# Optimization experiments

Hardware: AMD Instinct MI355X
Metric: run time of the kernel (lower is better)

The kernel has to match this reference:

```python
import jax, jax.numpy as jnp
import numpy as np

NUM_HEAD = 16
DIM_Q = 1024
DIM_K = 1024
DIM_KEY = 64
DIM_VAL = 64
EPS = 1e-6


def setup_inputs() -> dict:
    key = jax.random.key(0)
    ks = jax.random.split(key, 9)
    B, S = 4, 2048
    q = jax.random.normal(ks[0], (B, S, DIM_Q), dtype=jnp.float32)
    k = jax.random.normal(ks[1], (B, S, DIM_K), dtype=jnp.float32)
    v = jax.random.normal(ks[2], (B, S, DIM_K), dtype=jnp.float32)
    # Linear(in, out) weights stored as [out, in] like torch; applied as x @ W.T
    w_q = jax.random.normal(ks[3], (NUM_HEAD * DIM_KEY, DIM_Q), dtype=jnp.float32) * (1.0 / np.sqrt(DIM_Q))
    w_k = jax.random.normal(ks[4], (NUM_HEAD * DIM_KEY, DIM_K), dtype=jnp.float32) * (1.0 / np.sqrt(DIM_K))
    w_v = jax.random.normal(ks[5], (NUM_HEAD * DIM_KEY, DIM_K), dtype=jnp.float32) * (1.0 / np.sqrt(DIM_K))
    w_fc = jax.random.normal(ks[6], (DIM_Q, NUM_HEAD * DIM_VAL), dtype=jnp.float32) * (1.0 / np.sqrt(NUM_HEAD * DIM_VAL))
    ln_gamma = jnp.ones((DIM_Q,), dtype=jnp.float32)
    ln_beta = jnp.zeros((DIM_Q,), dtype=jnp.float32)
    return {"q": q, "k": k, "v": v, "w_q": w_q, "w_k": w_k, "w_v": w_v,
            "w_fc": w_fc, "ln_gamma": ln_gamma, "ln_beta": ln_beta}


def _layer_norm(x, gamma, beta):
    mu = jnp.mean(x, axis=-1, keepdims=True)
    var = jnp.mean(jnp.square(x - mu), axis=-1, keepdims=True)
    return (x - mu) * jax.lax.rsqrt(var + EPS) * gamma + beta


def reference(q, k, v, w_q, w_k, w_v, w_fc, ln_gamma, ln_beta):
    B, Sq, _ = q.shape
    Sk = k.shape[1]
    residual = q
    # projections -> [B, H, S, D]
    qh = (q @ w_q.T).reshape(B, Sq, NUM_HEAD, DIM_KEY).transpose(0, 2, 1, 3)
    kh = (k @ w_k.T).reshape(B, Sk, NUM_HEAD, DIM_KEY).transpose(0, 2, 1, 3)
    vh = (v @ w_v.T).reshape(B, Sk, NUM_HEAD, DIM_VAL).transpose(0, 2, 1, 3)
    scale = 1.0 / np.sqrt(DIM_KEY).astype(np.float32)
    attn = jax.nn.softmax(jnp.einsum('bhqd,bhkd->bhqk', qh, kh) * scale, axis=-1)
    out = jnp.einsum('bhqk,bhkd->bhqd', attn, vh)  # [B,H,Sq,Dv]
    out = out.transpose(0, 2, 1, 3).reshape(B, Sq, NUM_HEAD * DIM_VAL)
    out = out @ w_fc.T
    out = _layer_norm(out + residual, ln_gamma, ln_beta)
    return out, attn
```

## Files before the change

### kernel.cpp

```cpp
#include <hip/hip_runtime.h>


typedef __bf16 bf16_t;
typedef __bf16 bf16x4 __attribute__((ext_vector_type(4)));
typedef __bf16 bf16x8 __attribute__((ext_vector_type(8)));
typedef float f32x4 __attribute__((ext_vector_type(4)));

#define MFMA16(a, b, c) __builtin_amdgcn_mfma_f32_16x16x32_bf16((a), (b), (c), 0, 0, 0)

__global__ __launch_bounds__(256) void gemm_xwT(
    const float* __restrict__ A, const float* __restrict__ W,
    void* __restrict__ out, int mode, float scale)
{
    constexpr int K = 1024;
    __shared__ bf16_t As[128][72];
    __shared__ bf16_t Ws[128][72];

    const int t    = threadIdx.x;
    const int lane = t & 63;
    const int wv   = t >> 6;
    const int m0   = blockIdx.y * 128;
    const int n0   = blockIdx.x * 128;
    const int wr   = (wv >> 1) * 64;
    const int wc   = (wv & 1) * 64;

    f32x4 acc[4][4] = {};

    const int fr = lane & 15;
    const int fk = (lane >> 4) << 3;

    for (int k0 = 0; k0 < K; k0 += 64) {
        __syncthreads();
        for (int i = 0; i < 8; ++i) {
            int slot = t + i * 256;
            int r    = slot >> 4;
            int cg   = (slot & 15) << 2;
            float4 av = *(const float4*)(A + (size_t)(m0 + r) * K + k0 + cg);
            float4 wvv = *(const float4*)(W + (size_t)(n0 + r) * K + k0 + cg);
            bf16x4 ab, wb;
            ab[0] = (bf16_t)av.x;  ab[1] = (bf16_t)av.y;
            ab[2] = (bf16_t)av.z;  ab[3] = (bf16_t)av.w;
            wb[0] = (bf16_t)wvv.x; wb[1] = (bf16_t)wvv.y;
            wb[2] = (bf16_t)wvv.z; wb[3] = (bf16_t)wvv.w;
            *(bf16x4*)&As[r][cg] = ab;
            *(bf16x4*)&Ws[r][cg] = wb;
        }
        __syncthreads();
        for (int ks = 0; ks < 2; ++ks) {
            const int kk = ks * 32 + fk;
            bf16x8 af[4], bw[4];
            for (int i = 0; i < 4; ++i) af[i] = *(const bf16x8*)&As[wr + i * 16 + fr][kk];
            for (int j = 0; j < 4; ++j) bw[j] = *(const bf16x8*)&Ws[wc + j * 16 + fr][kk];
            for (int i = 0; i < 4; ++i)
                for (int j = 0; j < 4; ++j)
                    acc[i][j] = MFMA16(af[i], bw[j], acc[i][j]);
        }
    }

    const int cq = lane & 15;
    const int rq = (lane >> 4) << 2;
    for (int i = 0; i < 4; ++i) {
        for (int j = 0; j < 4; ++j) {
            const int n = n0 + wc + j * 16 + cq;
            for (int r = 0; r < 4; ++r) {
                const int m = m0 + wr + i * 16 + rq + r;
                const float v = acc[i][j][r] * scale;
                if (mode == 0) {
                    const int b = m >> 11, s = m & 2047;
                    const int h = n >> 6,  d = n & 63;
                    ((bf16_t*)out)[((size_t)((b * 16 + h) * 2048 + s) << 6) + d] = (bf16_t)v;
                } else {
                    ((float*)out)[(size_t)m * 1024 + n] = v;
                }
            }
        }
    }
}

__global__ __launch_bounds__(256) void attn_kernel(
    const bf16_t* __restrict__ qh, const bf16_t* __restrict__ kh,
    const bf16_t* __restrict__ vh, float* __restrict__ attn_out,
    float* __restrict__ o_out)
{
    __shared__ bf16_t Qs[64][72];
    __shared__ bf16_t Ks[128][72];
    __shared__ bf16_t Vt[64][136];
    __shared__ bf16_t Ps[64][136];
    __shared__ float  Linv[64];

    const int t    = threadIdx.x;
    const int lane = t & 63;
    const int wv   = t >> 6;
    const int qt   = blockIdx.x;
    const int bh   = blockIdx.y;
    const int sq0  = qt * 64;
    const size_t hbase = (size_t)bh * 2048 * 64;

    for (int i = 0; i < 2; ++i) {
        int slot = t + i * 256;
        int r = slot >> 3, g = (slot & 7) << 3;
        *(bf16x8*)&Qs[r][g] = *(const bf16x8*)(qh + hbase + (size_t)(sq0 + r) * 64 + g);
    }
    __syncthreads();

    const int fr    = lane & 15;
    const int fk    = (lane >> 4) << 3;
    const int rq    = (lane >> 4) << 2;
    const int rbase = wv * 16;

    const bf16x8 qa0 = *(const bf16x8*)&Qs[rbase + fr][fk];
    const bf16x8 qa1 = *(const bf16x8*)&Qs[rbase + fr][32 + fk];

    float lsum[4] = {0.f, 0.f, 0.f, 0.f};
    for (int kt = 0; kt < 16; ++kt) {
        __syncthreads();
        for (int i = 0; i < 4; ++i) {
            int slot = t + i * 256;
            int r = slot >> 3, g = (slot & 7) << 3;
            *(bf16x8*)&Ks[r][g] =
                *(const bf16x8*)(kh + hbase + (size_t)(kt * 128 + r) * 64 + g);
        }
        __syncthreads();
        for (int ct = 0; ct < 8; ++ct) {
            f32x4 c = {0.f, 0.f, 0.f, 0.f};
            bf16x8 b0 = *(const bf16x8*)&Ks[ct * 16 + fr][fk];
            bf16x8 b1 = *(const bf16x8*)&Ks[ct * 16 + fr][32 + fk];
            c = MFMA16(qa0, b0, c);
            c = MFMA16(qa1, b1, c);
            lsum[0] += __expf(c[0]); lsum[1] += __expf(c[1]);
            lsum[2] += __expf(c[2]); lsum[3] += __expf(c[3]);
        }
    }
    for (int m = 1; m < 16; m <<= 1)
        for (int r = 0; r < 4; ++r)
            lsum[r] += __shfl_xor(lsum[r], m, 64);
    if ((lane & 15) == 0)
        for (int r = 0; r < 4; ++r)
            Linv[rbase + rq + r] = 1.0f / lsum[r];
    __syncthreads();
    float inv[4];
    for (int r = 0; r < 4; ++r) inv[r] = Linv[rbase + rq + r];

    f32x4 oacc[4] = {};
    for (int kt = 0; kt < 16; ++kt) {
        __syncthreads();
        for (int i = 0; i < 4; ++i) {
            int slot = t + i * 256;
            int r = slot >> 3, g = (slot & 7) << 3;
            *(bf16x8*)&Ks[r][g] =
                *(const bf16x8*)(kh + hbase + (size_t)(kt * 128 + r) * 64 + g);
            int n = t & 127;
            int dvg = ((t >> 7) + 2 * i) << 3;
            bf16x8 vv = *(const bf16x8*)(vh + hbase + (size_t)(kt * 128 + n) * 64 + dvg);
            for (int j = 0; j < 8; ++j) Vt[dvg + j][n] = vv[j];
        }
        __syncthreads();
        for (int ct = 0; ct < 8; ++ct) {
            f32x4 c = {0.f, 0.f, 0.f, 0.f};
            bf16x8 b0 = *(const bf16x8*)&Ks[ct * 16 + fr][fk];
            bf16x8 b1 = *(const bf16x8*)&Ks[ct * 16 + fr][32 + fk];
            c = MFMA16(qa0, b0, c);
            c = MFMA16(qa1, b1, c);
            for (int r = 0; r < 4; ++r) {
                float p = __expf(c[r]) * inv[r];
                Ps[rbase + rq + r][ct * 16 + fr] = (bf16_t)p;
            }
        }
        __syncthreads();
        const size_t abase = ((size_t)bh * 2048 + sq0) * 2048 + kt * 128;
        for (int i = 0; i < 8; ++i) {
            int slot = t + i * 256;
            int r = slot >> 5, cg = (slot & 31) << 2;
            bf16x4 pv = *(const bf16x4*)&Ps[r][cg];
            float4 f;
            f.x = (float)pv[0]; f.y = (float)pv[1];
            f.z = (float)pv[2]; f.w = (float)pv[3];
            *(float4*)(attn_out + abase + (size_t)r * 2048 + cg) = f;
        }
        bf16x8 pa[4];
        for (int ks = 0; ks < 4; ++ks)
            pa[ks] = *(const bf16x8*)&Ps[rbase + fr][ks * 32 + fk];
        for (int dt = 0; dt < 4; ++dt)
            for (int ks = 0; ks < 4; ++ks) {
                bf16x8 bv = *(const bf16x8*)&Vt[dt * 16 + fr][ks * 32 + fk];
                oacc[dt] = MFMA16(pa[ks], bv, oacc[dt]);
            }
    }

    {
        const int b = bh >> 4, h = bh & 15;
        for (int dt = 0; dt < 4; ++dt)
            for (int r = 0; r < 4; ++r) {
                const int m = sq0 + rbase + rq + r;
                const int dv = dt * 16 + fr;
                o_out[(size_t)(b * 2048 + m) * 1024 + h * 64 + dv] = oacc[dt][r];
            }
    }
}

__global__ __launch_bounds__(256) void ln_kernel(
    const float* __restrict__ x, const float* __restrict__ resid,
    const float* __restrict__ gamma, const float* __restrict__ beta,
    float* __restrict__ out)
{
    const int row = blockIdx.x;
    const int t   = threadIdx.x;
    const size_t base = (size_t)row * 1024 + t * 4;
    float4 v = *(const float4*)(x + base);
    float4 rz = *(const float4*)(resid + base);
    v.x += rz.x; v.y += rz.y; v.z += rz.z; v.w += rz.w;
    float s  = v.x + v.y + v.z + v.w;
    float sq = v.x * v.x + v.y * v.y + v.z * v.z + v.w * v.w;
    for (int m = 1; m < 64; m <<= 1) {
        s  += __shfl_xor(s, m, 64);
        sq += __shfl_xor(sq, m, 64);
    }
    __shared__ float ws_s[4], ws_q[4];
    const int wv = t >> 6;
    if ((t & 63) == 0) { ws_s[wv] = s; ws_q[wv] = sq; }
    __syncthreads();
    s  = ws_s[0] + ws_s[1] + ws_s[2] + ws_s[3];
    sq = ws_q[0] + ws_q[1] + ws_q[2] + ws_q[3];
    const float mu  = s * (1.0f / 1024.0f);
    const float var = sq * (1.0f / 1024.0f) - mu * mu;
    const float rs  = rsqrtf(var + 1e-6f);
    float4 g = *(const float4*)(gamma + t * 4);
    float4 b = *(const float4*)(beta + t * 4);
    float4 y;
    y.x = (v.x - mu) * rs * g.x + b.x;
    y.y = (v.y - mu) * rs * g.y + b.y;
    y.z = (v.z - mu) * rs * g.z + b.z;
    y.w = (v.w - mu) * rs * g.w + b.w;
    *(float4*)(out + base) = y;
}

extern "C" void kernel_launch(void* const* d_in, const int* in_sizes, int n_in,
                              void* d_out, int out_size, void* d_ws, size_t ws_size,
                              hipStream_t stream)
{
    const float* q       = (const float*)d_in[0];
    const float* k       = (const float*)d_in[1];
    const float* v       = (const float*)d_in[2];
    const float* w_q     = (const float*)d_in[3];
    const float* w_k     = (const float*)d_in[4];
    const float* w_v     = (const float*)d_in[5];
    const float* w_fc    = (const float*)d_in[6];
    const float* ln_g    = (const float*)d_in[7];
    const float* ln_b    = (const float*)d_in[8];

    float* out      = (float*)d_out;
    float* attn_out = out + (size_t)4 * 2048 * 1024;

    char* ws = (char*)d_ws;
    bf16_t* qh    = (bf16_t*)(ws);
    bf16_t* kh    = (bf16_t*)(ws + (size_t)16777216);
    bf16_t* vh    = (bf16_t*)(ws + (size_t)33554432);
    float*  o_f32 = (float*)(ws + (size_t)50331648);
    float*  fc    = (float*)(ws);

    dim3 gg(8, 64);
    gemm_xwT<<<gg, 256, 0, stream>>>(q, w_q, qh, 0, 0.125f);
    gemm_xwT<<<gg, 256, 0, stream>>>(k, w_k, kh, 0, 1.0f);
    gemm_xwT<<<gg, 256, 0, stream>>>(v, w_v, vh, 0, 1.0f);

    attn_kernel<<<dim3(32, 64), 256, 0, stream>>>(qh, kh, vh, attn_out, o_f32);

    gemm_xwT<<<gg, 256, 0, stream>>>(o_f32, w_fc, fc, 1, 1.0f);

    ln_kernel<<<8192, 256, 0, stream>>>(fc, q, ln_g, ln_b, out);
}
```

Measured before the change: 1.545 ms.

## Enlarge attention query tile, pre-transpose V in projection, write attn directly from registers

The attention kernel now processes 128 query rows per block (32 per wave, two MFMA fragments), so each K/V tile loaded into shared memory is reused across twice as many queries. The V projection writes V already transposed (head, dim, seq), which removes the per-element scatter transpose into shared memory. Score MFMAs are issued with swapped operands so each lane holds four consecutive keys, letting attention probabilities be written to global memory as float4 directly from registers instead of through a shared-memory staging pass. The softmax row-sum reduction shrinks to two shuffles, and the Linv shared buffer and its barrier are removed. Loops are also explicitly unrolled. The larger tile raises register and LDS use per block and halves the grid, which may reduce occupancy.

Measured after the change: 1.683 ms. 1.09x slower.

```diff
diff --git a/kernel.cpp b/kernel.cpp
--- a/kernel.cpp
+++ b/kernel.cpp
@@ -31,11 +31,12 @@
 
     for (int k0 = 0; k0 < K; k0 += 64) {
         __syncthreads();
+        #pragma unroll
         for (int i = 0; i < 8; ++i) {
             int slot = t + i * 256;
             int r    = slot >> 4;
             int cg   = (slot & 15) << 2;
-            float4 av = *(const float4*)(A + (size_t)(m0 + r) * K + k0 + cg);
+            float4 av  = *(const float4*)(A + (size_t)(m0 + r) * K + k0 + cg);
             float4 wvv = *(const float4*)(W + (size_t)(n0 + r) * K + k0 + cg);
             bf16x4 ab, wb;
             ab[0] = (bf16_t)av.x;  ab[1] = (bf16_t)av.y;
@@ -46,12 +47,17 @@
             *(bf16x4*)&Ws[r][cg] = wb;
         }
         __syncthreads();
+        #pragma unroll
         for (int ks = 0; ks < 2; ++ks) {
             const int kk = ks * 32 + fk;
             bf16x8 af[4], bw[4];
+            #pragma unroll
             for (int i = 0; i < 4; ++i) af[i] = *(const bf16x8*)&As[wr + i * 16 + fr][kk];
+            #pragma unroll
             for (int j = 0; j < 4; ++j) bw[j] = *(const bf16x8*)&Ws[wc + j * 16 + fr][kk];
+            #pragma unroll
             for (int i = 0; i < 4; ++i)
+                #pragma unroll
                 for (int j = 0; j < 4; ++j)
                     acc[i][j] = MFMA16(af[i], bw[j], acc[i][j]);
         }
@@ -59,19 +65,32 @@
 
     const int cq = lane & 15;
     const int rq = (lane >> 4) << 2;
+    #pragma unroll
     for (int i = 0; i < 4; ++i) {
+        #pragma unroll
         for (int j = 0; j < 4; ++j) {
-            const int n = n0 + wc + j * 16 + cq;
-            for (int r = 0; r < 4; ++r) {
-                const int m = m0 + wr + i * 16 + rq + r;
-                const float v = acc[i][j][r] * scale;
-                if (mode == 0) {
+            const int n  = n0 + wc + j * 16 + cq;
+            const int mb = m0 + wr + i * 16 + rq;
+            if (mode == 0) {
+                const int h = n >> 6, d = n & 63;
+                #pragma unroll
+                for (int r = 0; r < 4; ++r) {
+                    const int m = mb + r;
                     const int b = m >> 11, s = m & 2047;
-                    const int h = n >> 6,  d = n & 63;
-                    ((bf16_t*)out)[((size_t)((b * 16 + h) * 2048 + s) << 6) + d] = (bf16_t)v;
-                } else {
-                    ((float*)out)[(size_t)m * 1024 + n] = v;
+                    ((bf16_t*)out)[((size_t)((b * 16 + h) * 2048 + s) << 6) + d] =
+                        (bf16_t)(acc[i][j][r] * scale);
                 }
+            } else if (mode == 1) {
+                #pragma unroll
+                for (int r = 0; r < 4; ++r)
+                    ((float*)out)[(size_t)(mb + r) * 1024 + n] = acc[i][j][r] * scale;
+            } else {
+                const int b = mb >> 11, s = mb & 2047;
+                const int h = n >> 6, d = n & 63;
+                bf16x4 pv;
+                #pragma unroll
+                for (int r = 0; r < 4; ++r) pv[r] = (bf16_t)(acc[i][j][r] * scale);
+                *(bf16x4*)((bf16_t*)out + (((size_t)(b * 16 + h) * 64 + d) << 11) + s) = pv;
             }
         }
     }
@@ -79,122 +98,147 @@
 
 __global__ __launch_bounds__(256) void attn_kernel(
     const bf16_t* __restrict__ qh, const bf16_t* __restrict__ kh,
-    const bf16_t* __restrict__ vh, float* __restrict__ attn_out,
+    const bf16_t* __restrict__ vt, float* __restrict__ attn_out,
     float* __restrict__ o_out)
 {
-    __shared__ bf16_t Qs[64][72];
     __shared__ bf16_t Ks[128][72];
     __shared__ bf16_t Vt[64][136];
-    __shared__ bf16_t Ps[64][136];
-    __shared__ float  Linv[64];
+    __shared__ bf16_t Ps[128][136];
 
     const int t    = threadIdx.x;
     const int lane = t & 63;
     const int wv   = t >> 6;
     const int qt   = blockIdx.x;
     const int bh   = blockIdx.y;
-    const int sq0  = qt * 64;
-    const size_t hbase = (size_t)bh * 2048 * 64;
-
-    for (int i = 0; i < 2; ++i) {
-        int slot = t + i * 256;
-        int r = slot >> 3, g = (slot & 7) << 3;
-        *(bf16x8*)&Qs[r][g] = *(const bf16x8*)(qh + hbase + (size_t)(sq0 + r) * 64 + g);
+    const int sq0  = qt * 128;
+    const size_t hbase  = (size_t)bh * 2048 * 64;
+    const size_t vtbase = (size_t)bh * 64 * 2048;
+
+    const int fr    = lane & 15;
+    const int quad  = lane >> 4;
+    const int fk    = quad << 3;
+    const int qbase = wv * 32;
+
+    {
+        const int r0 = t >> 3, g = (t & 7) << 3;
+        #pragma unroll
+        for (int i = 0; i < 4; ++i) {
+            int r = r0 + i * 32;
+            *(bf16x8*)&Ps[r][g] = *(const bf16x8*)(qh + hbase + (size_t)(sq0 + r) * 64 + g);
+        }
     }
     __syncthreads();
-
-    const int fr    = lane & 15;
-    const int fk    = (lane >> 4) << 3;
-    const int rq    = (lane >> 4) << 2;
-    const int rbase = wv * 16;
-
-    const bf16x8 qa0 = *(const bf16x8*)&Qs[rbase + fr][fk];
-    const bf16x8 qa1 = *(const bf16x8*)&Qs[rbase + fr][32 + fk];
-
-    float lsum[4] = {0.f, 0.f, 0.f, 0.f};
+    bf16x8 qa[2][2];
+    #pragma unroll
+    for (int f = 0; f < 2; ++f)
+        #pragma unroll
+        for (int h2 = 0; h2 < 2; ++h2)
+            qa[f][h2] = *(const bf16x8*)&Ps[qbase + f * 16 + fr][h2 * 32 + fk];
+
+    float lsum[2] = {0.f, 0.f};
     for (int kt = 0; kt < 16; ++kt) {
         __syncthreads();
-        for (int i = 0; i < 4; ++i) {
-            int slot = t + i * 256;
-            int r = slot >> 3, g = (slot & 7) << 3;
-            *(bf16x8*)&Ks[r][g] =
-                *(const bf16x8*)(kh + hbase + (size_t)(kt * 128 + r) * 64 + g);
-        }
-        __syncthreads();
+        {
+            const int r0 = t >> 3, g = (t & 7) << 3;
+            #pragma unroll
+            for (int i = 0; i < 4; ++i) {
+                int r = r0 + i * 32;
+                *(bf16x8*)&Ks[r][g] =
+                    *(const bf16x8*)(kh + hbase + (size_t)(kt * 128 + r) * 64 + g);
+            }
+        }
+        __syncthreads();
+        #pragma unroll
         for (int ct = 0; ct < 8; ++ct) {
-            f32x4 c = {0.f, 0.f, 0.f, 0.f};
             bf16x8 b0 = *(const bf16x8*)&Ks[ct * 16 + fr][fk];
             bf16x8 b1 = *(const bf16x8*)&Ks[ct * 16 + fr][32 + fk];
-            c = MFMA16(qa0, b0, c);
-            c = MFMA16(qa1, b1, c);
-            lsum[0] += __expf(c[0]); lsum[1] += __expf(c[1]);
-            lsum[2] += __expf(c[2]); lsum[3] += __expf(c[3]);
-        }
-    }
-    for (int m = 1; m < 16; m <<= 1)
-        for (int r = 0; r < 4; ++r)
-            lsum[r] += __shfl_xor(lsum[r], m, 64);
-    if ((lane & 15) == 0)
-        for (int r = 0; r < 4; ++r)
-            Linv[rbase + rq + r] = 1.0f / lsum[r];
-    __syncthreads();
-    float inv[4];
-    for (int r = 0; r < 4; ++r) inv[r] = Linv[rbase + rq + r];
-
-    f32x4 oacc[4] = {};
+            #pragma unroll
+            for (int f = 0; f < 2; ++f) {
+                f32x4 c = {0.f, 0.f, 0.f, 0.f};
+                c = MFMA16(b0, qa[f][0], c);
+                c = MFMA16(b1, qa[f][1], c);
+                lsum[f] += __expf(c[0]) + __expf(c[1]) + __expf(c[2]) + __expf(c[3]);
+            }
+        }
+    }
+    float inv[2];
+    #pragma unroll
+    for (int f = 0; f < 2; ++f) {
+        float s = lsum[f];
+        s += __shfl_xor(s, 16, 64);
+        s += __shfl_xor(s, 32, 64);
+        inv[f] = 1.0f / s;
+    }
+
+    f32x4 oacc[2][4] = {};
     for (int kt = 0; kt < 16; ++kt) {
         __syncthreads();
-        for (int i = 0; i < 4; ++i) {
-            int slot = t + i * 256;
-            int r = slot >> 3, g = (slot & 7) << 3;
-            *(bf16x8*)&Ks[r][g] =
-                *(const bf16x8*)(kh + hbase + (size_t)(kt * 128 + r) * 64 + g);
-            int n = t & 127;
-            int dvg = ((t >> 7) + 2 * i) << 3;
-            bf16x8 vv = *(const bf16x8*)(vh + hbase + (size_t)(kt * 128 + n) * 64 + dvg);
-            for (int j = 0; j < 8; ++j) Vt[dvg + j][n] = vv[j];
-        }
-        __syncthreads();
+        {
+            const int r0 = t >> 3, g = (t & 7) << 3;
+            #pragma unroll
+            for (int i = 0; i < 4; ++i) {
+                int r = r0 + i * 32;
+                *(bf16x8*)&Ks[r][g] =
+                    *(const bf16x8*)(kh + hbase + (size_t)(kt * 128 + r) * 64 + g);
+            }
+            const int vr0 = t >> 4, vg = (t & 15) << 3;
+            #pragma unroll
+            for (int i = 0; i < 4; ++i) {
+                int r = vr0 + i * 16;
+                *(bf16x8*)&Vt[r][vg] =
+                    *(const bf16x8*)(vt + vtbase + (size_t)r * 2048 + kt * 128 + vg);
+            }
+        }
+        __syncthreads();
+        const size_t arow0 = ((size_t)bh * 2048 + sq0 + qbase + fr) * 2048
+                           + (size_t)kt * 128 + quad * 4;
+        #pragma unroll
         for (int ct = 0; ct < 8; ++ct) {
-            f32x4 c = {0.f, 0.f, 0.f, 0.f};
             bf16x8 b0 = *(const bf16x8*)&Ks[ct * 16 + fr][fk];
             bf16x8 b1 = *(const bf16x8*)&Ks[ct * 16 + fr][32 + fk];
-            c = MFMA16(qa0, b0, c);
-            c = MFMA16(qa1, b1, c);
-            for (int r = 0; r < 4; ++r) {
-                float p = __expf(c[r]) * inv[r];
-                Ps[rbase + rq + r][ct * 16 + fr] = (bf16_t)p;
-            }
-        }
-        __syncthreads();
-        const size_t abase = ((size_t)bh * 2048 + sq0) * 2048 + kt * 128;
-        for (int i = 0; i < 8; ++i) {
-            int slot = t + i * 256;
-            int r = slot >> 5, cg = (slot & 31) << 2;
-            bf16x4 pv = *(const bf16x4*)&Ps[r][cg];
-            float4 f;
-            f.x = (float)pv[0]; f.y = (float)pv[1];
-            f.z = (float)pv[2]; f.w = (float)pv[3];
-            *(float4*)(attn_out + abase + (size_t)r * 2048 + cg) = f;
-        }
-        bf16x8 pa[4];
-        for (int ks = 0; ks < 4; ++ks)
-            pa[ks] = *(const bf16x8*)&Ps[rbase + fr][ks * 32 + fk];
-        for (int dt = 0; dt < 4; ++dt)
-            for (int ks = 0; ks < 4; ++ks) {
+            #pragma unroll
+            for (int f = 0; f < 2; ++f) {
+                f32x4 c = {0.f, 0.f, 0.f, 0.f};
+                c = MFMA16(b0, qa[f][0], c);
+                c = MFMA16(b1, qa[f][1], c);
+                float4 p;
+                p.x = __expf(c[0]) * inv[f];
+                p.y = __expf(c[1]) * inv[f];
+                p.z = __expf(c[2]) * inv[f];
+                p.w = __expf(c[3]) * inv[f];
+                *(float4*)(attn_out + arow0 + (size_t)f * 16 * 2048 + ct * 16) = p;
+                bf16x4 pb;
+                pb[0] = (bf16_t)p.x; pb[1] = (bf16_t)p.y;
+                pb[2] = (bf16_t)p.z; pb[3] = (bf16_t)p.w;
+                *(bf16x4*)&Ps[qbase + f * 16 + fr][ct * 16 + quad * 4] = pb;
+            }
+        }
+        #pragma unroll
+        for (int ks = 0; ks < 4; ++ks) {
+            bf16x8 pa0 = *(const bf16x8*)&Ps[qbase + fr][ks * 32 + fk];
+            bf16x8 pa1 = *(const bf16x8*)&Ps[qbase + 16 + fr][ks * 32 + fk];
+            #pragma unroll
+            for (int dt = 0; dt < 4; ++dt) {
                 bf16x8 bv = *(const bf16x8*)&Vt[dt * 16 + fr][ks * 32 + fk];
-                oacc[dt] = MFMA16(pa[ks], bv, oacc[dt]);
-            }
+                oacc[0][dt] = MFMA16(pa0, bv, oacc[0][dt]);
+                oacc[1][dt] = MFMA16(pa1, bv, oacc[1][dt]);
+            }
+        }
     }
 
     {
         const int b = bh >> 4, h = bh & 15;
-        for (int dt = 0; dt < 4; ++dt)
-            for (int r = 0; r < 4; ++r) {
-                const int m = sq0 + rbase + rq + r;
-                const int dv = dt * 16 + fr;
-                o_out[(size_t)(b * 2048 + m) * 1024 + h * 64 + dv] = oacc[dt][r];
-            }
+        const int rq = quad << 2;
+        #pragma unroll
+        for (int f = 0; f < 2; ++f)
+            #pragma unroll
+            for (int dt = 0; dt < 4; ++dt)
+                #pragma unroll
+                for (int r = 0; r < 4; ++r) {
+                    const int m = sq0 + qbase + f * 16 + rq + r;
+                    o_out[(size_t)(b * 2048 + m) * 1024 + h * 64 + dt * 16 + fr] =
+                        oacc[f][dt][r];
+                }
     }
 }
 
@@ -206,7 +250,7 @@
     const int row = blockIdx.x;
     const int t   = threadIdx.x;
     const size_t base = (size_t)row * 1024 + t * 4;
-    float4 v = *(const float4*)(x + base);
+    float4 v  = *(const float4*)(x + base);
     float4 rz = *(const float4*)(resid + base);
     v.x += rz.x; v.y += rz.y; v.z += rz.z; v.w += rz.w;
     float s  = v.x + v.y + v.z + v.w;
@@ -238,15 +282,15 @@
                               void* d_out, int out_size, void* d_ws, size_t ws_size,
                               hipStream_t stream)
 {
-    const float* q       = (const float*)d_in[0];
-    const float* k       = (const float*)d_in[1];
-    const float* v       = (const float*)d_in[2];
-    const float* w_q     = (const float*)d_in[3];
-    const float* w_k     = (const float*)d_in[4];
-    const float* w_v     = (const float*)d_in[5];
-    const float* w_fc    = (const float*)d_in[6];
-    const float* ln_g    = (const float*)d_in[7];
-    const float* ln_b    = (const float*)d_in[8];
+    const float* q    = (const float*)d_in[0];
+    const float* k    = (const float*)d_in[1];
+    const float* v    = (const float*)d_in[2];
+    const float* w_q  = (const float*)d_in[3];
+    const float* w_k  = (const float*)d_in[4];
+    const float* w_v  = (const float*)d_in[5];
+    const float* w_fc = (const float*)d_in[6];
+    const float* ln_g = (const float*)d_in[7];
+    const float* ln_b = (const float*)d_in[8];
 
     float* out      = (float*)d_out;
     float* attn_out = out + (size_t)4 * 2048 * 1024;
@@ -254,16 +298,16 @@
     char* ws = (char*)d_ws;
     bf16_t* qh    = (bf16_t*)(ws);
     bf16_t* kh    = (bf16_t*)(ws + (size_t)16777216);
-    bf16_t* vh    = (bf16_t*)(ws + (size_t)33554432);
+    bf16_t* vt    = (bf16_t*)(ws + (size_t)33554432);
     float*  o_f32 = (float*)(ws + (size_t)50331648);
     float*  fc    = (float*)(ws);
 
     dim3 gg(8, 64);
     gemm_xwT<<<gg, 256, 0, stream>>>(q, w_q, qh, 0, 0.125f);
     gemm_xwT<<<gg, 256, 0, stream>>>(k, w_k, kh, 0, 1.0f);
-    gemm_xwT<<<gg, 256, 0, stream>>>(v, w_v, vh, 0, 1.0f);
-
-    attn_kernel<<<dim3(32, 64), 256, 0, stream>>>(qh, kh, vh, attn_out, o_f32);
+    gemm_xwT<<<gg, 256, 0, stream>>>(v, w_v, vt, 2, 1.0f);
+
+    attn_kernel<<<dim3(16, 64), 256, 0, stream>>>(qh, kh, vt, attn_out, o_f32);
 
     gemm_xwT<<<gg, 256, 0, stream>>>(o_f32, w_fc, fc, 1, 1.0f);
 
```
